# Performance work log

Measured on AMD Instinct MI355X. Metric: run time of the kernel, lower is better.

The kernel has to match this reference:

```python
import jax, jax.numpy as jnp
import numpy as np

NEG_SLOPE = 0.2
EPS = 1e-16

N_NODES = 50000
N_EDGES = 800000
N_QUERY = 100000


def setup_inputs() -> dict:
    key = jax.random.key(0)
    ks = jax.random.split(key, 12)
    x = jax.random.normal(ks[0], (N_NODES, 128), dtype=jnp.float32)
    edge_index = jax.random.randint(ks[1], (2, N_EDGES), 0, N_NODES, dtype=jnp.int64)
    edge_label_index = jax.random.randint(ks[2], (2, N_QUERY), 0, N_NODES, dtype=jnp.int64)
    # layer 1: in=128 -> out=256, heads=4, per-head dim 64
    W1 = jax.random.normal(ks[3], (128, 256), dtype=jnp.float32) * 0.08
    a1_src = jax.random.normal(ks[4], (4, 64), dtype=jnp.float32) * 0.08
    a1_dst = jax.random.normal(ks[5], (4, 64), dtype=jnp.float32) * 0.08
    b1 = jnp.zeros((256,), dtype=jnp.float32)
    # layer 2: in=256 -> out=32, heads=2, per-head dim 16
    W2 = jax.random.normal(ks[6], (256, 32), dtype=jnp.float32) * 0.08
    a2_src = jax.random.normal(ks[7], (2, 16), dtype=jnp.float32) * 0.08
    a2_dst = jax.random.normal(ks[8], (2, 16), dtype=jnp.float32) * 0.08
    b2 = jnp.zeros((32,), dtype=jnp.float32)
    return {"x": x, "edge_index": edge_index, "edge_label_index": edge_label_index,
            "W1": W1, "a1_src": a1_src, "a1_dst": a1_dst, "b1": b1,
            "W2": W2, "a2_src": a2_src, "a2_dst": a2_dst, "b2": b2}


def gat_layer(x, src, dst, W, a_src, a_dst, b, heads):
    """Multi-head GAT: gather -> edge logits -> segment softmax over dst -> scatter-add."""
    n = x.shape[0]
    out = W.shape[1]
    c = out // heads
    h = (x @ W).reshape(n, heads, c)                       # [N,H,C]
    # per-node attention contributions: [N,H]
    alpha_s = jnp.einsum('nhc,hc->nh', h, a_src)
    alpha_d = jnp.einsum('nhc,hc->nh', h, a_dst)
    e = alpha_s[src] + alpha_d[dst]                         # [E,H]
    e = jax.nn.leaky_relu(e, NEG_SLOPE)
    # segment softmax over incoming edges of each dst node
    m = jax.ops.segment_max(e, dst, num_segments=n)         # [N,H]
    m = jnp.where(jnp.isfinite(m), m, 0.0)
    ex = jnp.exp(e - m[dst])                                # [E,H]
    s = jax.ops.segment_sum(ex, dst, num_segments=n)        # [N,H]
    w = ex / (s[dst] + EPS)                                 # [E,H]
    msg = h[src] * w[:, :, None]                            # [E,H,C]
    agg = jax.ops.segment_sum(msg, dst, num_segments=n)     # [N,H,C]
    return agg.reshape(n, out) + b


def reference(x, edge_index, edge_label_index, W1, a1_src, a1_dst, b1, W2, a2_src, a2_dst, b2):
    n = x.shape[0]
    loops = jnp.arange(n, dtype=edge_index.dtype)
    src = jnp.concatenate([edge_index[0], loops])
    dst = jnp.concatenate([edge_index[1], loops])
    # encode (dropout p=0 and use_bn=False are identities)
    z = gat_layer(x, src, dst, W1, a1_src, a1_dst, b1, heads=4)
    z = jax.nn.relu(z)
    z = gat_layer(z, src, dst, W2, a2_src, a2_dst, b2, heads=2)
    # decode: dot product of endpoint embeddings
    return (z[edge_label_index[0]] * z[edge_label_index[1]]).sum(axis=-1)
```

## Files before the change

### kernel.cpp

```cpp
#include <hip/hip_runtime.h>

#define NEG_SLOPE 0.2f
#define EPSV 1e-16f

__global__ void k_deg(const int* __restrict__ ei, int E, int N, int* __restrict__ deg){
  int t = blockIdx.x*blockDim.x + threadIdx.x;
  int ET = E + N;
  if (t >= ET) return;
  int dst = (t < E) ? ei[E + t] : (t - E);
  atomicAdd(&deg[dst], 1);
}

__global__ void k_scan(const int* __restrict__ deg, int N, int* __restrict__ rs){
  __shared__ int sums[1024];
  int tid = threadIdx.x;
  int chunk = (N + 1023) >> 10;
  int s = tid*chunk, e = min(s+chunk, N);
  int sum = 0;
  for (int i = s; i < e; ++i) sum += deg[i];
  sums[tid] = sum;
  __syncthreads();
  for (int off = 1; off < 1024; off <<= 1){
    int v = (tid >= off) ? sums[tid-off] : 0;
    __syncthreads();
    sums[tid] += v;
    __syncthreads();
  }
  int run = (tid == 0) ? 0 : sums[tid-1];
  for (int i = s; i < e; ++i){ rs[i] = run; run += deg[i]; }
  if (tid == 1023) rs[N] = run;
}

__global__ void k_fill(const int* __restrict__ ei, int E, int N,
                       const int* __restrict__ rs, int* __restrict__ cnt,
                       int* __restrict__ csr_s){
  int t = blockIdx.x*blockDim.x + threadIdx.x;
  int ET = E + N;
  if (t >= ET) return;
  int src, dst;
  if (t < E){ src = ei[t]; dst = ei[E + t]; } else { src = dst = t - E; }
  int pos = atomicAdd(&cnt[dst], 1);
  csr_s[rs[dst] + pos] = src;
}

__global__ __launch_bounds__(256) void k_gemm1(const float* __restrict__ x, const float* __restrict__ W1,
                                               const float* __restrict__ a1s, const float* __restrict__ a1d,
                                               int N, float* __restrict__ h1,
                                               float* __restrict__ als, float* __restrict__ ald){
  __shared__ float xs[8][128];
  int bn = blockIdx.x * 8;
  int tid = threadIdx.x;
  {
    int m = tid >> 5, k4 = tid & 31;
    int node = bn + m;
    float4 v = (node < N) ? ((const float4*)x)[(size_t)node*32 + k4]
                          : make_float4(0.f,0.f,0.f,0.f);
    ((float4*)xs[m])[k4] = v;
  }
  __syncthreads();
  float acc[8];
  #pragma unroll
  for (int m = 0; m < 8; ++m) acc[m] = 0.f;
  int j = tid;
  for (int k = 0; k < 128; ++k){
    float w = W1[k*256 + j];
    #pragma unroll
    for (int m = 0; m < 8; ++m) acc[m] = fmaf(xs[m][k], w, acc[m]);
  }
  int head = j >> 6;
  int lane = j & 63;
  float cas = a1s[head*64 + lane];
  float cad = a1d[head*64 + lane];
  #pragma unroll
  for (int m = 0; m < 8; ++m){
    int node = bn + m;
    if (node < N) h1[(size_t)node*256 + j] = acc[m];
    float vs = acc[m]*cas, vd = acc[m]*cad;
    #pragma unroll
    for (int o = 32; o; o >>= 1){ vs += __shfl_xor(vs, o, 64); vd += __shfl_xor(vd, o, 64); }
    if (lane == 0 && node < N){ als[node*4+head] = vs; ald[node*4+head] = vd; }
  }
}

__global__ __launch_bounds__(256) void k_gemm2(const float* __restrict__ z1, const float* __restrict__ W2,
                                               const float* __restrict__ a2s, const float* __restrict__ a2d,
                                               int N, float* __restrict__ h2,
                                               float* __restrict__ als, float* __restrict__ ald){
  __shared__ float zs[8][256];
  int bn = blockIdx.x * 8;
  int tid = threadIdx.x;
  {
    int m = tid >> 6, k4 = tid & 63;
    int node = bn + m;
    const float4 zero = make_float4(0.f,0.f,0.f,0.f);
    ((float4*)zs[m])[k4]      = (node < N)   ? ((const float4*)z1)[(size_t)node*64 + k4] : zero;
    int m2 = m + 4, node2 = bn + m2;
    ((float4*)zs[m2])[k4]     = (node2 < N)  ? ((const float4*)z1)[(size_t)node2*64 + k4] : zero;
  }
  __syncthreads();
  int j = tid & 31;
  int m = tid >> 5;
  float acc = 0.f;
  for (int k = 0; k < 256; ++k) acc = fmaf(zs[m][k], W2[k*32 + j], acc);
  int node = bn + m;
  int head = j >> 4, lane = j & 15;
  if (node < N) h2[(size_t)node*32 + j] = acc;
  float vs = acc * a2s[head*16 + lane];
  float vd = acc * a2d[head*16 + lane];
  #pragma unroll
  for (int o = 8; o; o >>= 1){ vs += __shfl_xor(vs, o, 64); vd += __shfl_xor(vd, o, 64); }
  if (lane == 0 && node < N){ als[node*2+head] = vs; ald[node*2+head] = vd; }
}

__device__ __forceinline__ float lrelu(float e){ return (e > 0.f) ? e : NEG_SLOPE*e; }

__global__ __launch_bounds__(256) void k_agg1(const int* __restrict__ rs, const int* __restrict__ csr_s,
                                              const float* __restrict__ als, const float* __restrict__ ald,
                                              const float* __restrict__ h1, const float* __restrict__ b1,
                                              int N, float* __restrict__ z1){
  int node = blockIdx.x;
  int tid = threadIdx.x;
  int head = tid >> 6;
  float aldn = ald[node*4 + head];
  int beg = rs[node], end = rs[node+1];
  float acc = 0.f, s = 0.f;
  int i = beg;
  for (; i + 3 < end; i += 4){
    int s0 = csr_s[i], s1 = csr_s[i+1], s2 = csr_s[i+2], s3 = csr_s[i+3];
    float x0 = __expf(lrelu(als[s0*4+head] + aldn));
    float x1 = __expf(lrelu(als[s1*4+head] + aldn));
    float x2 = __expf(lrelu(als[s2*4+head] + aldn));
    float x3 = __expf(lrelu(als[s3*4+head] + aldn));
    float v0 = h1[(size_t)s0*256 + tid];
    float v1 = h1[(size_t)s1*256 + tid];
    float v2 = h1[(size_t)s2*256 + tid];
    float v3 = h1[(size_t)s3*256 + tid];
    acc = fmaf(v0, x0, acc); acc = fmaf(v1, x1, acc);
    acc = fmaf(v2, x2, acc); acc = fmaf(v3, x3, acc);
    s += (x0 + x1) + (x2 + x3);
  }
  for (; i < end; ++i){
    int s0 = csr_s[i];
    float x0 = __expf(lrelu(als[s0*4+head] + aldn));
    acc = fmaf(h1[(size_t)s0*256 + tid], x0, acc);
    s += x0;
  }
  float v = acc / (s + EPSV) + b1[tid];
  z1[(size_t)node*256 + tid] = v > 0.f ? v : 0.f;
}

__global__ __launch_bounds__(256) void k_agg2(const int* __restrict__ rs, const int* __restrict__ csr_s,
                                              const float* __restrict__ als, const float* __restrict__ ald,
                                              const float* __restrict__ h2, const float* __restrict__ b2,
                                              int N, float* __restrict__ z2){
  int tid = threadIdx.x;
  int node = blockIdx.x*4 + (tid >> 6);
  if (node >= N) return;
  int lane = tid & 63;
  int slot = lane >> 5;
  int c    = lane & 31;
  int head = c >> 4;
  float aldn = ald[node*2 + head];
  int beg = rs[node], end = rs[node+1];
  float acc = 0.f, s = 0.f;
  int i = beg + slot;
  for (; i + 2 < end; i += 4){
    int s0 = csr_s[i], s1 = csr_s[i+2];
    float x0 = __expf(lrelu(als[s0*2+head] + aldn));
    float x1 = __expf(lrelu(als[s1*2+head] + aldn));
    float v0 = h2[(size_t)s0*32 + c];
    float v1 = h2[(size_t)s1*32 + c];
    acc = fmaf(v0, x0, acc); acc = fmaf(v1, x1, acc);
    s += x0 + x1;
  }
  if (i < end){
    int s0 = csr_s[i];
    float x0 = __expf(lrelu(als[s0*2+head] + aldn));
    acc = fmaf(h2[(size_t)s0*32 + c], x0, acc);
    s += x0;
  }
  acc += __shfl_xor(acc, 32, 64);
  s   += __shfl_xor(s,   32, 64);
  if (slot == 0)
    z2[(size_t)node*32 + c] = acc / (s + EPSV) + b2[c];
}

__global__ void k_decode(const int* __restrict__ eli, int NQ,
                         const float* __restrict__ z2, float* __restrict__ out){
  int t = blockIdx.x*blockDim.x + threadIdx.x;
  if (t >= NQ*32) return;
  int q = t >> 5, c = t & 31;
  int a = eli[q], b = eli[NQ + q];
  float p = z2[(size_t)a*32 + c] * z2[(size_t)b*32 + c];
  #pragma unroll
  for (int o = 16; o; o >>= 1) p += __shfl_xor(p, o, 64);
  if (c == 0) out[q] = p;
}

extern "C" void kernel_launch(void* const* d_in, const int* in_sizes, int n_in,
                              void* d_out, int out_size, void* d_ws, size_t ws_size,
                              hipStream_t stream) {
  const float* x   = (const float*)d_in[0];
  const int*   ei  = (const int*)d_in[1];
  const int*   eli = (const int*)d_in[2];
  const float* W1  = (const float*)d_in[3];
  const float* a1s = (const float*)d_in[4];
  const float* a1d = (const float*)d_in[5];
  const float* b1  = (const float*)d_in[6];
  const float* W2  = (const float*)d_in[7];
  const float* a2s = (const float*)d_in[8];
  const float* a2d = (const float*)d_in[9];
  const float* b2  = (const float*)d_in[10];
  float* out = (float*)d_out;

  int N  = in_sizes[0] / 128;
  int E  = in_sizes[1] / 2;
  int NQ = in_sizes[2] / 2;
  int ET = E + N;

  char* base = (char*)d_ws;
  size_t off = 0;
  auto alloc = [&](size_t elems)->char*{ char* r = base + off; off += elems*4; return r; };
  int*   deg   = (int*)  alloc(N);
  int*   cnt   = (int*)  alloc(N);
  size_t zbytes = off;
  int*   rs    = (int*)  alloc(N+1);
  int*   csr_s = (int*)  alloc(ET);
  float* al1s  = (float*)alloc((size_t)N*4);
  float* al1d  = (float*)alloc((size_t)N*4);
  float* al2s  = (float*)alloc((size_t)N*2);
  float* al2d  = (float*)alloc((size_t)N*2);
  float* h1    = (float*)alloc((size_t)N*256);
  float* z1    = (float*)alloc((size_t)N*256);
  float* h2    = (float*)alloc((size_t)N*32);
  float* z2    = (float*)alloc((size_t)N*32);
  (void)ws_size; (void)n_in; (void)out_size;

  hipMemsetAsync(d_ws, 0, zbytes, stream);

  k_deg <<<(ET+255)/256, 256, 0, stream>>>(ei, E, N, deg);
  k_scan<<<1, 1024, 0, stream>>>(deg, N, rs);
  k_fill<<<(ET+255)/256, 256, 0, stream>>>(ei, E, N, rs, cnt, csr_s);

  k_gemm1<<<(N+7)/8, 256, 0, stream>>>(x, W1, a1s, a1d, N, h1, al1s, al1d);
  k_agg1<<<N, 256, 0, stream>>>(rs, csr_s, al1s, al1d, h1, b1, N, z1);

  k_gemm2<<<(N+7)/8, 256, 0, stream>>>(z1, W2, a2s, a2d, N, h2, al2s, al2d);
  k_agg2<<<(N+3)/4, 256, 0, stream>>>(rs, csr_s, al2s, al2d, h2, b2, N, z2);

  k_decode<<<((long long)NQ*32+255)/256, 256, 0, stream>>>(eli, NQ, z2, out);
}
```

Baseline: 556.3 us.

## Vectorize GAT aggregation with float4 loads and split edges across wavefronts

Layer-1 aggregation now has each of the four wavefronts handle a strided subset of a node's incoming edges, with float4 loads covering the full 256-wide row. Partial sums are reduced through shared memory. This cuts per-edge softmax-weight computation and index loads, and raises memory-level parallelism. Layer-2 aggregation and decode also move to float4 loads, with more edge slots per wave and shuffle reductions. The cost is an extra shared-memory reduction and barrier per node, and only one wave does the final write.

After: 540.9 us. -2.8%, faster.

```diff
diff --git a/kernel.cpp b/kernel.cpp
--- a/kernel.cpp
+++ b/kernel.cpp
@@ -2,6 +2,8 @@
 
 #define NEG_SLOPE 0.2f
 #define EPSV 1e-16f
+
+__device__ __forceinline__ float lrelu(float e){ return (e > 0.f) ? e : NEG_SLOPE*e; }
 
 __global__ void k_deg(const int* __restrict__ ei, int E, int N, int* __restrict__ deg){
   int t = blockIdx.x*blockDim.x + threadIdx.x;
@@ -112,41 +114,58 @@
   if (lane == 0 && node < N){ als[node*2+head] = vs; ald[node*2+head] = vd; }
 }
 
-__device__ __forceinline__ float lrelu(float e){ return (e > 0.f) ? e : NEG_SLOPE*e; }
-
 __global__ __launch_bounds__(256) void k_agg1(const int* __restrict__ rs, const int* __restrict__ csr_s,
                                               const float* __restrict__ als, const float* __restrict__ ald,
                                               const float* __restrict__ h1, const float* __restrict__ b1,
                                               int N, float* __restrict__ z1){
+  __shared__ float4 accl[4][64];
+  __shared__ float  sl[4][64];
   int node = blockIdx.x;
   int tid = threadIdx.x;
-  int head = tid >> 6;
+  int w = tid >> 6, lane = tid & 63;
+  int head = lane >> 4;
   float aldn = ald[node*4 + head];
   int beg = rs[node], end = rs[node+1];
-  float acc = 0.f, s = 0.f;
-  int i = beg;
-  for (; i + 3 < end; i += 4){
-    int s0 = csr_s[i], s1 = csr_s[i+1], s2 = csr_s[i+2], s3 = csr_s[i+3];
+  float4 acc = make_float4(0.f,0.f,0.f,0.f);
+  float s = 0.f;
+  int i = beg + w;
+  for (; i + 4 < end; i += 8){
+    int s0 = csr_s[i], s1 = csr_s[i+4];
     float x0 = __expf(lrelu(als[s0*4+head] + aldn));
     float x1 = __expf(lrelu(als[s1*4+head] + aldn));
-    float x2 = __expf(lrelu(als[s2*4+head] + aldn));
-    float x3 = __expf(lrelu(als[s3*4+head] + aldn));
-    float v0 = h1[(size_t)s0*256 + tid];
-    float v1 = h1[(size_t)s1*256 + tid];
-    float v2 = h1[(size_t)s2*256 + tid];
-    float v3 = h1[(size_t)s3*256 + tid];
-    acc = fmaf(v0, x0, acc); acc = fmaf(v1, x1, acc);
-    acc = fmaf(v2, x2, acc); acc = fmaf(v3, x3, acc);
-    s += (x0 + x1) + (x2 + x3);
-  }
-  for (; i < end; ++i){
+    float4 v0 = ((const float4*)h1)[(size_t)s0*64 + lane];
+    float4 v1 = ((const float4*)h1)[(size_t)s1*64 + lane];
+    acc.x = fmaf(v0.x, x0, acc.x); acc.y = fmaf(v0.y, x0, acc.y);
+    acc.z = fmaf(v0.z, x0, acc.z); acc.w = fmaf(v0.w, x0, acc.w);
+    acc.x = fmaf(v1.x, x1, acc.x); acc.y = fmaf(v1.y, x1, acc.y);
+    acc.z = fmaf(v1.z, x1, acc.z); acc.w = fmaf(v1.w, x1, acc.w);
+    s += x0 + x1;
+  }
+  if (i < end){
     int s0 = csr_s[i];
     float x0 = __expf(lrelu(als[s0*4+head] + aldn));
-    acc = fmaf(h1[(size_t)s0*256 + tid], x0, acc);
+    float4 v0 = ((const float4*)h1)[(size_t)s0*64 + lane];
+    acc.x = fmaf(v0.x, x0, acc.x); acc.y = fmaf(v0.y, x0, acc.y);
+    acc.z = fmaf(v0.z, x0, acc.z); acc.w = fmaf(v0.w, x0, acc.w);
     s += x0;
   }
-  float v = acc / (s + EPSV) + b1[tid];
-  z1[(size_t)node*256 + tid] = v > 0.f ? v : 0.f;
+  accl[w][lane] = acc;
+  sl[w][lane] = s;
+  __syncthreads();
+  if (tid < 64){
+    float4 a0 = accl[0][tid], a1 = accl[1][tid], a2 = accl[2][tid], a3 = accl[3][tid];
+    float st = sl[0][tid] + sl[1][tid] + sl[2][tid] + sl[3][tid];
+    float inv = 1.0f / (st + EPSV);
+    float4 bb = ((const float4*)b1)[tid];
+    float4 r;
+    r.x = fmaf(a0.x + a1.x + a2.x + a3.x, inv, bb.x);
+    r.y = fmaf(a0.y + a1.y + a2.y + a3.y, inv, bb.y);
+    r.z = fmaf(a0.z + a1.z + a2.z + a3.z, inv, bb.z);
+    r.w = fmaf(a0.w + a1.w + a2.w + a3.w, inv, bb.w);
+    r.x = fmaxf(r.x, 0.f); r.y = fmaxf(r.y, 0.f);
+    r.z = fmaxf(r.z, 0.f); r.w = fmaxf(r.w, 0.f);
+    ((float4*)z1)[(size_t)node*64 + tid] = r;
+  }
 }
 
 __global__ __launch_bounds__(256) void k_agg2(const int* __restrict__ rs, const int* __restrict__ csr_s,
@@ -157,44 +176,48 @@
   int node = blockIdx.x*4 + (tid >> 6);
   if (node >= N) return;
   int lane = tid & 63;
-  int slot = lane >> 5;
-  int c    = lane & 31;
-  int head = c >> 4;
+  int slot = lane >> 3;
+  int q    = lane & 7;
+  int head = q >> 2;
   float aldn = ald[node*2 + head];
   int beg = rs[node], end = rs[node+1];
-  float acc = 0.f, s = 0.f;
-  int i = beg + slot;
-  for (; i + 2 < end; i += 4){
-    int s0 = csr_s[i], s1 = csr_s[i+2];
-    float x0 = __expf(lrelu(als[s0*2+head] + aldn));
-    float x1 = __expf(lrelu(als[s1*2+head] + aldn));
-    float v0 = h2[(size_t)s0*32 + c];
-    float v1 = h2[(size_t)s1*32 + c];
-    acc = fmaf(v0, x0, acc); acc = fmaf(v1, x1, acc);
-    s += x0 + x1;
-  }
-  if (i < end){
+  float4 acc = make_float4(0.f,0.f,0.f,0.f);
+  float s = 0.f;
+  for (int i = beg + slot; i < end; i += 8){
     int s0 = csr_s[i];
     float x0 = __expf(lrelu(als[s0*2+head] + aldn));
-    acc = fmaf(h2[(size_t)s0*32 + c], x0, acc);
+    float4 v0 = ((const float4*)h2)[(size_t)s0*8 + q];
+    acc.x = fmaf(v0.x, x0, acc.x); acc.y = fmaf(v0.y, x0, acc.y);
+    acc.z = fmaf(v0.z, x0, acc.z); acc.w = fmaf(v0.w, x0, acc.w);
     s += x0;
   }
-  acc += __shfl_xor(acc, 32, 64);
-  s   += __shfl_xor(s,   32, 64);
-  if (slot == 0)
-    z2[(size_t)node*32 + c] = acc / (s + EPSV) + b2[c];
+  #pragma unroll
+  for (int o = 8; o < 64; o <<= 1){
+    acc.x += __shfl_xor(acc.x, o, 64); acc.y += __shfl_xor(acc.y, o, 64);
+    acc.z += __shfl_xor(acc.z, o, 64); acc.w += __shfl_xor(acc.w, o, 64);
+    s += __shfl_xor(s, o, 64);
+  }
+  if (slot == 0){
+    float inv = 1.0f / (s + EPSV);
+    float4 bb = ((const float4*)b2)[q];
+    float4 r;
+    r.x = fmaf(acc.x, inv, bb.x); r.y = fmaf(acc.y, inv, bb.y);
+    r.z = fmaf(acc.z, inv, bb.z); r.w = fmaf(acc.w, inv, bb.w);
+    ((float4*)z2)[(size_t)node*8 + q] = r;
+  }
 }
 
 __global__ void k_decode(const int* __restrict__ eli, int NQ,
                          const float* __restrict__ z2, float* __restrict__ out){
   int t = blockIdx.x*blockDim.x + threadIdx.x;
-  if (t >= NQ*32) return;
-  int q = t >> 5, c = t & 31;
-  int a = eli[q], b = eli[NQ + q];
-  float p = z2[(size_t)a*32 + c] * z2[(size_t)b*32 + c];
-  #pragma unroll
-  for (int o = 16; o; o >>= 1) p += __shfl_xor(p, o, 64);
-  if (c == 0) out[q] = p;
+  if (t >= NQ*8) return;
+  int qq = t >> 3, q = t & 7;
+  int a = eli[qq], b = eli[NQ + qq];
+  float4 va = ((const float4*)z2)[(size_t)a*8 + q];
+  float4 vb = ((const float4*)z2)[(size_t)b*8 + q];
+  float p = va.x*vb.x + va.y*vb.y + va.z*vb.z + va.w*vb.w;
+  p += __shfl_xor(p, 1, 64); p += __shfl_xor(p, 2, 64); p += __shfl_xor(p, 4, 64);
+  if (q == 0) out[qq] = p;
 }
 
 extern "C" void kernel_launch(void* const* d_in, const int* in_sizes, int n_in,
@@ -248,5 +271,5 @@
   k_gemm2<<<(N+7)/8, 256, 0, stream>>>(z1, W2, a2s, a2d, N, h2, al2s, al2d);
   k_agg2<<<(N+3)/4, 256, 0, stream>>>(rs, csr_s, al2s, al2d, h2, b2, N, z2);
 
-  k_decode<<<((long long)NQ*32+255)/256, 256, 0, stream>>>(eli, NQ, z2, out);
-}
+  k_decode<<<((long long)NQ*8+255)/256, 256, 0, stream>>>(eli, NQ, z2, out);
+}
```
